# Optimization experiments

Hardware: AMD Instinct MI355X
Metric: run time of the kernel (lower is better)

The kernel has to match this reference:

```python
import jax, jax.numpy as jnp
import numpy as np

B, N_ATOMS, D_ATOM = 64, 256, 256
T_ANGLES = 2048
D_HID, D_OUT = 512, 256
BN_EPS = 1e-5


def setup_inputs() -> dict:
    key = jax.random.key(0)
    ks = jax.random.split(key, 8)
    z = jax.random.normal(ks[0], (B, N_ATOMS, D_ATOM), dtype=jnp.float32)
    # all entries valid (>=0) so the nonzero-selected row set is all B*T rows
    angel_atom_table = jax.random.randint(ks[1], (B, T_ANGLES, 3), 0, N_ATOMS, dtype=jnp.int64)
    W1 = jax.random.normal(ks[2], (D_ATOM, D_HID), dtype=jnp.float32) * (1.0 / np.sqrt(D_ATOM))
    b1 = jax.random.normal(ks[3], (D_HID,), dtype=jnp.float32) * 0.01
    gamma = jnp.ones((D_HID,), dtype=jnp.float32)
    beta = jnp.zeros((D_HID,), dtype=jnp.float32)
    W2 = jax.random.normal(ks[4], (D_HID, D_OUT), dtype=jnp.float32) * (1.0 / np.sqrt(D_HID))
    b2 = jax.random.normal(ks[5], (D_OUT,), dtype=jnp.float32) * 0.01
    return {"z": z, "angel_atom_table": angel_atom_table, "W1": W1, "b1": b1,
            "gamma": gamma, "beta": beta, "W2": W2, "b2": b2}


def reference(z, angel_atom_table, W1, b1, gamma, beta, W2, b2):
    Bb, Tt, _ = angel_atom_table.shape
    bi = jnp.arange(Bb)[:, None]                       # [B,1] broadcast batch index
    # gather 3 atom embeddings per angle and sum -> [B,T,d_atom]
    x = (z[bi, angel_atom_table[:, :, 0]]
         + z[bi, angel_atom_table[:, :, 1]]
         + z[bi, angel_atom_table[:, :, 2]])
    x = x.reshape(Bb * Tt, -1)                         # flattened valid rows (all valid)
    h = x @ W1 + b1                                    # Linear(d_atom, d_hid)
    mean = jnp.mean(h, axis=0)                         # BatchNorm1d (batch stats)
    var = jnp.var(h, axis=0)
    h = (h - mean) * jax.lax.rsqrt(var + BN_EPS) * gamma + beta
    h = jax.nn.relu(h)                                 # dropout inactive (eval)
    out = h @ W2 + b2                                  # Linear(d_hid, d_output)
    return out
```

## Files before the change

kernel.cpp:

```cpp
#include <hip/hip_runtime.h>

static constexpr int Bn  = 64;
static constexpr int T   = 2048;
static constexpr int NA  = 256;
static constexpr int DA  = 256;
static constexpr int DH  = 512;
static constexpr int DO  = 256;
static constexpr int M   = Bn * T;
static constexpr int NBS = M / 128;
static constexpr int NBC = M / 64;

typedef __attribute__((ext_vector_type(4))) float  f32x4;
typedef __attribute__((ext_vector_type(8))) __bf16 bf16x8;
typedef __attribute__((ext_vector_type(8))) short  short8;

__device__ __forceinline__ unsigned short f2bf(float f) {
  union { float f; unsigned u; } v; v.f = f;
  unsigned u = v.u + 0x7FFFu + ((v.u >> 16) & 1u);
  return (unsigned short)(u >> 16);
}
__device__ __forceinline__ float bf2f(unsigned short b) {
  union { unsigned u; float f; } v; v.u = ((unsigned)b) << 16;
  return v.f;
}

__global__ void prep_kernel(const float* __restrict__ W1, const float* __restrict__ W2,
                            unsigned short* __restrict__ W1T, unsigned short* __restrict__ W2T) {
  int id = blockIdx.x * 256 + threadIdx.x;
  {
    int n = id >> 8, k = id & 255;
    W1T[id] = f2bf(W1[k * DH + n]);
  }
  {
    int n = id >> 9, k = id & 511;
    W2T[id] = f2bf(W2[k * DO + n]);
  }
}

__global__ __launch_bounds__(512, 4) void kA_zw(
    const float* __restrict__ z, const unsigned short* __restrict__ W1T,
    unsigned short* __restrict__ zW) {
  __shared__ __align__(16) unsigned short As[32][64][8];
  const int tid = threadIdx.x;
  const int xcd = blockIdx.x & 7, idx = blockIdx.x >> 3;
  const int bm = xcd * 32 + (idx >> 1), bn = idx & 1;
  const int row0 = bm * 64, n0b = bn * 256;
  const int wave = tid >> 6, lane = tid & 63, ql = lane >> 4, r16 = lane & 15;
  const int gq = tid >> 8, t8 = tid & 255;
  const int gr = t8 >> 2, sub = t8 & 3;
  const int sxw = (sub << 2) ^ sub;
  const int sxr = (ql << 2) ^ ql;

  const unsigned short* bp = W1T + (size_t)(n0b + wave * 32 + r16) * DA + ql * 8;

  bf16x8 bq[2][2];
#pragma unroll
  for (int p = 0; p < 2; ++p)
#pragma unroll
    for (int nf = 0; nf < 2; ++nf)
      bq[p][nf] = *(const bf16x8*)(bp + nf * 16 * DA + p * 32);

  {
    const float* zr = z + (size_t)(row0 + gr) * DA + sub * 8;
#pragma unroll
    for (int cl = 0; cl < 4; ++cl) {
      const int cg = gq * 4 + cl;
      f32x4 a0 = *(const f32x4*)(zr + cg * 32);
      f32x4 a1 = *(const f32x4*)(zr + cg * 32 + 4);
      bf16x8 pk;
#pragma unroll
      for (int j = 0; j < 4; ++j) { pk[j] = (__bf16)a0[j]; pk[4 + j] = (__bf16)a1[j]; }
      *(bf16x8*)&As[cg * 4 + sub][gr ^ sxw][0] = pk;
    }
  }
  __syncthreads();

  f32x4 acc[4][2] = {};
#pragma unroll
  for (int s = 0; s < 8; ++s) {
    bf16x8 afr[4], bfr[2];
#pragma unroll
    for (int mf = 0; mf < 4; ++mf)
      afr[mf] = *(const bf16x8*)&As[s * 4 + ql][(mf * 16 + r16) ^ sxr][0];
#pragma unroll
    for (int nf = 0; nf < 2; ++nf) bfr[nf] = bq[s & 1][nf];
    __builtin_amdgcn_s_setprio(1);
#pragma unroll
    for (int mf = 0; mf < 4; ++mf)
#pragma unroll
      for (int nf = 0; nf < 2; ++nf)
        acc[mf][nf] = __builtin_amdgcn_mfma_f32_16x16x32_bf16(afr[mf], bfr[nf], acc[mf][nf], 0, 0, 0);
    __builtin_amdgcn_s_setprio(0);
    if (s + 2 < 8) {
#pragma unroll
      for (int nf = 0; nf < 2; ++nf)
        bq[s & 1][nf] = *(const bf16x8*)(bp + nf * 16 * DA + (s + 2) * 32);
    }
  }

  const int n0 = n0b + wave * 32;
#pragma unroll
  for (int nf = 0; nf < 2; ++nf) {
    const int col = n0 + nf * 16 + r16;
#pragma unroll
    for (int mf = 0; mf < 4; ++mf)
#pragma unroll
      for (int p = 0; p < 4; ++p)
        zW[(size_t)(row0 + mf * 16 + ql * 4 + p) * DH + col] = f2bf(acc[mf][nf][p]);
  }
}

__global__ __launch_bounds__(256) void kB_stats(
    const unsigned short* __restrict__ zW, const int* __restrict__ tbl,
    float* __restrict__ psum, float* __restrict__ psq) {
  __shared__ int idxs[128][3];
  __shared__ float red1[4][512];
  __shared__ float red2[4][512];
  const int bid = blockIdx.x;
  const int blk = (bid & 7) * (NBS >> 3) + (bid >> 3);
  const int tid = threadIdx.x;
  const int row0 = blk * 128;
  const unsigned short* zWb = zW + (size_t)(row0 >> 11) * NA * DH;

  for (int i = tid; i < 384; i += 256) ((int*)idxs)[i] = tbl[(size_t)row0 * 3 + i];
  __syncthreads();

  const int cc = tid & 63, rg = tid >> 6;
  float s1[8] = {0, 0, 0, 0, 0, 0, 0, 0};
  float s2[8] = {0, 0, 0, 0, 0, 0, 0, 0};
#pragma unroll 8
  for (int i = 0; i < 32; ++i) {
    const int r = rg * 32 + i;
    const unsigned short* p0 = zWb + (size_t)idxs[r][0] * DH + cc * 8;
    const unsigned short* p1 = zWb + (size_t)idxs[r][1] * DH + cc * 8;
    const unsigned short* p2 = zWb + (size_t)idxs[r][2] * DH + cc * 8;
    short8 v0 = *(const short8*)p0;
    short8 v1 = *(const short8*)p1;
    short8 v2 = *(const short8*)p2;
#pragma unroll
    for (int j = 0; j < 8; ++j) {
      float h = bf2f((unsigned short)v0[j]) + bf2f((unsigned short)v1[j]) + bf2f((unsigned short)v2[j]);
      s1[j] += h;
      s2[j] = fmaf(h, h, s2[j]);
    }
  }
#pragma unroll
  for (int j = 0; j < 8; ++j) { red1[rg][cc * 8 + j] = s1[j]; red2[rg][cc * 8 + j] = s2[j]; }
  __syncthreads();
  for (int c = tid; c < 512; c += 256) {
    psum[(size_t)c * NBS + blk] = red1[0][c] + red1[1][c] + red1[2][c] + red1[3][c];
    psq [(size_t)c * NBS + blk] = red2[0][c] + red2[1][c] + red2[2][c] + red2[3][c];
  }
}

__global__ void k2_stats(const float* __restrict__ psum, const float* __restrict__ psq,
                         const float* __restrict__ gamma, const float* __restrict__ beta,
                         float* __restrict__ coef) {
  const int col = blockIdx.x, lane = threadIdx.x;
  float s1 = 0.f, s2 = 0.f;
  for (int i = lane; i < NBS; i += 64) {
    s1 += psum[(size_t)col * NBS + i];
    s2 += psq [(size_t)col * NBS + i];
  }
#pragma unroll
  for (int d = 1; d < 64; d <<= 1) { s1 += __shfl_xor(s1, d); s2 += __shfl_xor(s2, d); }
  if (lane == 0) {
    const float inv = 1.0f / (float)M;
    float mean = s1 * inv;
    float var  = s2 * inv - mean * mean;
    float a = gamma[col] * rsqrtf(var + 1e-5f);
    coef[col]      = a;
    coef[DH + col] = beta[col] - mean * a;
  }
}

__global__ __launch_bounds__(512, 4) void kC_out(
    const unsigned short* __restrict__ zW, const int* __restrict__ tbl,
    const unsigned short* __restrict__ W2T, const float* __restrict__ coef,
    const float* __restrict__ b2, float* __restrict__ out) {
  __shared__ __align__(16) unsigned short As[32][64][8];
  __shared__ float aC[DH], dC[DH];
  __shared__ int idxs[64][3];

  const int bid = blockIdx.x;
  const int blk = (bid & 7) * (NBC >> 3) + (bid >> 3);
  const int tid = threadIdx.x;
  const int row0 = blk * 64;
  const unsigned short* zWb = zW + (size_t)(row0 >> 11) * NA * DH;

  if (tid < 192) ((int*)idxs)[tid] = tbl[(size_t)row0 * 3 + tid];
  aC[tid] = coef[tid];
  dC[tid] = coef[DH + tid];
  __syncthreads();

  const int wave = tid >> 6, lane = tid & 63, ql = lane >> 4, r16 = lane & 15;
  const int gq = tid >> 8, t8 = tid & 255;
  const int gr = t8 >> 2, sub = t8 & 3;
  const int sxw = (sub << 2) ^ sub;
  const int sxr = (ql << 2) ^ ql;

  const unsigned short* g0p = zWb + (size_t)idxs[gr][0] * DH + sub * 8;
  const unsigned short* g1p = zWb + (size_t)idxs[gr][1] * DH + sub * 8;
  const unsigned short* g2p = zWb + (size_t)idxs[gr][2] * DH + sub * 8;

  const unsigned short* bp = W2T + (size_t)(wave * 32 + r16) * DH + ql * 8;

  bf16x8 bq[2][2];
#pragma unroll
  for (int p = 0; p < 2; ++p)
#pragma unroll
    for (int nf = 0; nf < 2; ++nf)
      bq[p][nf] = *(const bf16x8*)(bp + nf * 16 * DH + p * 32);

  f32x4 acc[4][2] = {};

#pragma unroll
  for (int h = 0; h < 2; ++h) {
    if (h) __builtin_amdgcn_s_barrier();
#pragma unroll
    for (int cl = 0; cl < 4; ++cl) {
      const int coff = h * 256 + (gq * 4 + cl) * 32;
      short8 v0 = *(const short8*)(g0p + coff);
      short8 v1 = *(const short8*)(g1p + coff);
      short8 v2 = *(const short8*)(g2p + coff);
      const int kk = coff + sub * 8;
      f32x4 av0 = *(const f32x4*)&aC[kk];
      f32x4 av1 = *(const f32x4*)&aC[kk + 4];
      f32x4 dv0 = *(const f32x4*)&dC[kk];
      f32x4 dv1 = *(const f32x4*)&dC[kk + 4];
      bf16x8 pk;
#pragma unroll
      for (int j = 0; j < 4; ++j) {
        float h0 = bf2f((unsigned short)v0[j]) + bf2f((unsigned short)v1[j]) + bf2f((unsigned short)v2[j]);
        float f0 = fmaf(h0, av0[j], dv0[j]);
        f0 = f0 > 0.f ? f0 : 0.f;
        pk[j] = (__bf16)f0;
        float h1 = bf2f((unsigned short)v0[4 + j]) + bf2f((unsigned short)v1[4 + j]) + bf2f((unsigned short)v2[4 + j]);
        float f1 = fmaf(h1, av1[j], dv1[j]);
        f1 = f1 > 0.f ? f1 : 0.f;
        pk[4 + j] = (__bf16)f1;
      }
      *(bf16x8*)&As[(gq * 4 + cl) * 4 + sub][gr ^ sxw][0] = pk;
    }
    asm volatile("s_waitcnt lgkmcnt(0)" ::: "memory");
    __builtin_amdgcn_s_barrier();
    __builtin_amdgcn_sched_barrier(0);

#pragma unroll
    for (int s = 0; s < 8; ++s) {
      const int sg = h * 8 + s;
      bf16x8 afr[4], bfr[2];
#pragma unroll
      for (int mf = 0; mf < 4; ++mf)
        afr[mf] = *(const bf16x8*)&As[s * 4 + ql][(mf * 16 + r16) ^ sxr][0];
#pragma unroll
      for (int nf = 0; nf < 2; ++nf) bfr[nf] = bq[sg & 1][nf];
      __builtin_amdgcn_s_setprio(1);
#pragma unroll
      for (int mf = 0; mf < 4; ++mf)
#pragma unroll
        for (int nf = 0; nf < 2; ++nf)
          acc[mf][nf] = __builtin_amdgcn_mfma_f32_16x16x32_bf16(afr[mf], bfr[nf], acc[mf][nf], 0, 0, 0);
      __builtin_amdgcn_s_setprio(0);
      if (sg + 2 < 16) {
#pragma unroll
        for (int nf = 0; nf < 2; ++nf)
          bq[sg & 1][nf] = *(const bf16x8*)(bp + nf * 16 * DH + (sg + 2) * 32);
      }
    }
  }

  const int n0 = wave * 32;
#pragma unroll
  for (int nf = 0; nf < 2; ++nf) {
    const int col = n0 + nf * 16 + r16;
    const float bv = b2[col];
#pragma unroll
    for (int mf = 0; mf < 4; ++mf)
#pragma unroll
      for (int p = 0; p < 4; ++p)
        out[(size_t)(row0 + mf * 16 + ql * 4 + p) * DO + col] = acc[mf][nf][p] + bv;
  }
}

extern "C" void kernel_launch(void* const* d_in, const int* in_sizes, int n_in,
                              void* d_out, int out_size, void* d_ws, size_t ws_size,
                              hipStream_t stream) {
  const float* z     = (const float*)d_in[0];
  const int*   tbl   = (const int*)d_in[1];
  const float* W1    = (const float*)d_in[2];
  const float* gamma = (const float*)d_in[4];
  const float* beta  = (const float*)d_in[5];
  const float* W2    = (const float*)d_in[6];
  const float* b2    = (const float*)d_in[7];
  float* out = (float*)d_out;

  char* ws = (char*)d_ws;
  unsigned short* W1T  = (unsigned short*)(ws);
  unsigned short* W2T  = (unsigned short*)(ws + (256 << 10));
  float*          coef = (float*)(ws + (512 << 10));
  float*          psum = (float*)(ws + (2 << 20));
  float*          psq  = (float*)(ws + (4 << 20));
  unsigned short* zW   = (unsigned short*)(ws + (16 << 20));

  prep_kernel<<<512, 256, 0, stream>>>(W1, W2, W1T, W2T);
  kA_zw<<<512, 512, 0, stream>>>(z, W1T, zW);
  kB_stats<<<NBS, 256, 0, stream>>>(zW, tbl, psum, psq);
  k2_stats<<<DH, 64, 0, stream>>>(psum, psq, gamma, beta, coef);
  kC_out<<<NBC, 512, 0, stream>>>(zW, tbl, W2T, coef, b2, out);
}
```

Measured before the change: 268.5 us.

## Prefetch gathered rows into registers and overlap second-half gather with MFMA

```diff
diff --git a/kernel.cpp b/kernel.cpp
--- a/kernel.cpp
+++ b/kernel.cpp
@@ -180,7 +180,6 @@
     const float* __restrict__ b2, float* __restrict__ out) {
   __shared__ __align__(16) unsigned short As[32][64][8];
   __shared__ float aC[DH], dC[DH];
-  __shared__ int idxs[64][3];
 
   const int bid = blockIdx.x;
   const int blk = (bid & 7) * (NBC >> 3) + (bid >> 3);
@@ -188,98 +187,160 @@
   const int row0 = blk * 64;
   const unsigned short* zWb = zW + (size_t)(row0 >> 11) * NA * DH;
 
-  if (tid < 192) ((int*)idxs)[tid] = tbl[(size_t)row0 * 3 + tid];
   aC[tid] = coef[tid];
   dC[tid] = coef[DH + tid];
+
+  const int gr = tid >> 3, sc = tid & 7;
+  const size_t tb = (size_t)(row0 + gr) * 3;
+  const int i0 = tbl[tb], i1 = tbl[tb + 1], i2 = tbl[tb + 2];
+  const unsigned short* g0p = zWb + (size_t)i0 * DH + sc * 8;
+  const unsigned short* g1p = zWb + (size_t)i1 * DH + sc * 8;
+  const unsigned short* g2p = zWb + (size_t)i2 * DH + sc * 8;
+
+  short8 a0[4], a1[4], a2[4];
+#pragma unroll
+  for (int it = 0; it < 4; ++it) {
+    a0[it] = *(const short8*)(g0p + it * 64);
+    a1[it] = *(const short8*)(g1p + it * 64);
+    a2[it] = *(const short8*)(g2p + it * 64);
+  }
+
+  const int wave = tid >> 6, lane = tid & 63, ql = lane >> 4, r16 = lane & 15;
+  const int rg2 = wave >> 2;
+  const int cg  = wave & 3;
+
+  const unsigned short* bp = W2T + (size_t)(cg * 64 + r16) * DH + ql * 8;
+  bf16x8 bq[2][4];
+#pragma unroll
+  for (int p = 0; p < 2; ++p)
+#pragma unroll
+    for (int nf = 0; nf < 4; ++nf)
+      bq[p][nf] = *(const bf16x8*)(bp + nf * 16 * DH + p * 32);
+
   __syncthreads();
 
-  const int wave = tid >> 6, lane = tid & 63, ql = lane >> 4, r16 = lane & 15;
-  const int gq = tid >> 8, t8 = tid & 255;
-  const int gr = t8 >> 2, sub = t8 & 3;
-  const int sxw = (sub << 2) ^ sub;
-  const int sxr = (ql << 2) ^ ql;
-
-  const unsigned short* g0p = zWb + (size_t)idxs[gr][0] * DH + sub * 8;
-  const unsigned short* g1p = zWb + (size_t)idxs[gr][1] * DH + sub * 8;
-  const unsigned short* g2p = zWb + (size_t)idxs[gr][2] * DH + sub * 8;
-
-  const unsigned short* bp = W2T + (size_t)(wave * 32 + r16) * DH + ql * 8;
-
-  bf16x8 bq[2][2];
-#pragma unroll
-  for (int p = 0; p < 2; ++p)
-#pragma unroll
-    for (int nf = 0; nf < 2; ++nf)
-      bq[p][nf] = *(const bf16x8*)(bp + nf * 16 * DH + p * 32);
-
-  f32x4 acc[4][2] = {};
-
-#pragma unroll
-  for (int h = 0; h < 2; ++h) {
-    if (h) __builtin_amdgcn_s_barrier();
-#pragma unroll
-    for (int cl = 0; cl < 4; ++cl) {
-      const int coff = h * 256 + (gq * 4 + cl) * 32;
-      short8 v0 = *(const short8*)(g0p + coff);
-      short8 v1 = *(const short8*)(g1p + coff);
-      short8 v2 = *(const short8*)(g2p + coff);
-      const int kk = coff + sub * 8;
-      f32x4 av0 = *(const f32x4*)&aC[kk];
-      f32x4 av1 = *(const f32x4*)&aC[kk + 4];
-      f32x4 dv0 = *(const f32x4*)&dC[kk];
-      f32x4 dv1 = *(const f32x4*)&dC[kk + 4];
-      bf16x8 pk;
-#pragma unroll
-      for (int j = 0; j < 4; ++j) {
-        float h0 = bf2f((unsigned short)v0[j]) + bf2f((unsigned short)v1[j]) + bf2f((unsigned short)v2[j]);
-        float f0 = fmaf(h0, av0[j], dv0[j]);
-        f0 = f0 > 0.f ? f0 : 0.f;
-        pk[j] = (__bf16)f0;
-        float h1 = bf2f((unsigned short)v0[4 + j]) + bf2f((unsigned short)v1[4 + j]) + bf2f((unsigned short)v2[4 + j]);
-        float f1 = fmaf(h1, av1[j], dv1[j]);
-        f1 = f1 > 0.f ? f1 : 0.f;
-        pk[4 + j] = (__bf16)f1;
-      }
-      *(bf16x8*)&As[(gq * 4 + cl) * 4 + sub][gr ^ sxw][0] = pk;
-    }
-    asm volatile("s_waitcnt lgkmcnt(0)" ::: "memory");
-    __builtin_amdgcn_s_barrier();
-    __builtin_amdgcn_sched_barrier(0);
-
-#pragma unroll
-    for (int s = 0; s < 8; ++s) {
-      const int sg = h * 8 + s;
-      bf16x8 afr[4], bfr[2];
-#pragma unroll
-      for (int mf = 0; mf < 4; ++mf)
-        afr[mf] = *(const bf16x8*)&As[s * 4 + ql][(mf * 16 + r16) ^ sxr][0];
-#pragma unroll
-      for (int nf = 0; nf < 2; ++nf) bfr[nf] = bq[sg & 1][nf];
-      __builtin_amdgcn_s_setprio(1);
-#pragma unroll
-      for (int mf = 0; mf < 4; ++mf)
-#pragma unroll
-        for (int nf = 0; nf < 2; ++nf)
-          acc[mf][nf] = __builtin_amdgcn_mfma_f32_16x16x32_bf16(afr[mf], bfr[nf], acc[mf][nf], 0, 0, 0);
-      __builtin_amdgcn_s_setprio(0);
-      if (sg + 2 < 16) {
-#pragma unroll
-        for (int nf = 0; nf < 2; ++nf)
-          bq[sg & 1][nf] = *(const bf16x8*)(bp + nf * 16 * DH + (sg + 2) * 32);
-      }
-    }
-  }
-
-  const int n0 = wave * 32;
-#pragma unroll
-  for (int nf = 0; nf < 2; ++nf) {
-    const int col = n0 + nf * 16 + r16;
+#pragma unroll
+  for (int it = 0; it < 4; ++it) {
+    const int kk = it * 64 + sc * 8;
+    f32x4 av0 = *(const f32x4*)&aC[kk];
+    f32x4 av1 = *(const f32x4*)&aC[kk + 4];
+    f32x4 dv0 = *(const f32x4*)&dC[kk];
+    f32x4 dv1 = *(const f32x4*)&dC[kk + 4];
+    bf16x8 pk;
+#pragma unroll
+    for (int j = 0; j < 4; ++j) {
+      float h0 = bf2f((unsigned short)a0[it][j]) + bf2f((unsigned short)a1[it][j]) + bf2f((unsigned short)a2[it][j]);
+      float f0 = fmaf(h0, av0[j], dv0[j]);
+      f0 = f0 > 0.f ? f0 : 0.f;
+      pk[j] = (__bf16)f0;
+      float h1 = bf2f((unsigned short)a0[it][4 + j]) + bf2f((unsigned short)a1[it][4 + j]) + bf2f((unsigned short)a2[it][4 + j]);
+      float f1 = fmaf(h1, av1[j], dv1[j]);
+      f1 = f1 > 0.f ? f1 : 0.f;
+      pk[4 + j] = (__bf16)f1;
+    }
+    *(bf16x8*)&As[it * 8 + sc][gr ^ sc][0] = pk;
+  }
+
+  short8 p0[4], p1[4];
+#pragma unroll
+  for (int it = 0; it < 4; ++it) {
+    p0[it] = *(const short8*)(g0p + 256 + it * 64);
+    p1[it] = *(const short8*)(g1p + 256 + it * 64);
+  }
+
+  asm volatile("s_waitcnt lgkmcnt(0)" ::: "memory");
+  __builtin_amdgcn_s_barrier();
+  __builtin_amdgcn_sched_barrier(0);
+
+  f32x4 acc[2][4] = {};
+
+#pragma unroll
+  for (int s = 0; s < 8; ++s) {
+    const int swz = ((s & 1) << 2) | ql;
+    bf16x8 afr[2], bfr[4];
+#pragma unroll
+    for (int mf = 0; mf < 2; ++mf)
+      afr[mf] = *(const bf16x8*)&As[s * 4 + ql][(rg2 * 32 + mf * 16 + r16) ^ swz][0];
+#pragma unroll
+    for (int nf = 0; nf < 4; ++nf) bfr[nf] = bq[s & 1][nf];
+    __builtin_amdgcn_s_setprio(1);
+#pragma unroll
+    for (int mf = 0; mf < 2; ++mf)
+#pragma unroll
+      for (int nf = 0; nf < 4; ++nf)
+        acc[mf][nf] = __builtin_amdgcn_mfma_f32_16x16x32_bf16(afr[mf], bfr[nf], acc[mf][nf], 0, 0, 0);
+    __builtin_amdgcn_s_setprio(0);
+#pragma unroll
+    for (int nf = 0; nf < 4; ++nf)
+      bq[s & 1][nf] = *(const bf16x8*)(bp + nf * 16 * DH + (s + 2) * 32);
+  }
+
+  __builtin_amdgcn_s_barrier();
+
+  short8 p2[4];
+#pragma unroll
+  for (int it = 0; it < 4; ++it)
+    p2[it] = *(const short8*)(g2p + 256 + it * 64);
+
+#pragma unroll
+  for (int it = 0; it < 4; ++it) {
+    const int kk = 256 + it * 64 + sc * 8;
+    f32x4 av0 = *(const f32x4*)&aC[kk];
+    f32x4 av1 = *(const f32x4*)&aC[kk + 4];
+    f32x4 dv0 = *(const f32x4*)&dC[kk];
+    f32x4 dv1 = *(const f32x4*)&dC[kk + 4];
+    bf16x8 pk;
+#pragma unroll
+    for (int j = 0; j < 4; ++j) {
+      float h0 = bf2f((unsigned short)p0[it][j]) + bf2f((unsigned short)p1[it][j]) + bf2f((unsigned short)p2[it][j]);
+      float f0 = fmaf(h0, av0[j], dv0[j]);
+      f0 = f0 > 0.f ? f0 : 0.f;
+      pk[j] = (__bf16)f0;
+      float h1 = bf2f((unsigned short)p0[it][4 + j]) + bf2f((unsigned short)p1[it][4 + j]) + bf2f((unsigned short)p2[it][4 + j]);
+      float f1 = fmaf(h1, av1[j], dv1[j]);
+      f1 = f1 > 0.f ? f1 : 0.f;
+      pk[4 + j] = (__bf16)f1;
+    }
+    *(bf16x8*)&As[it * 8 + sc][gr ^ sc][0] = pk;
+  }
+  asm volatile("s_waitcnt lgkmcnt(0)" ::: "memory");
+  __builtin_amdgcn_s_barrier();
+  __builtin_amdgcn_sched_barrier(0);
+
+#pragma unroll
+  for (int s = 0; s < 8; ++s) {
+    const int sg = 8 + s;
+    const int swz = ((s & 1) << 2) | ql;
+    bf16x8 afr[2], bfr[4];
+#pragma unroll
+    for (int mf = 0; mf < 2; ++mf)
+      afr[mf] = *(const bf16x8*)&As[s * 4 + ql][(rg2 * 32 + mf * 16 + r16) ^ swz][0];
+#pragma unroll
+    for (int nf = 0; nf < 4; ++nf) bfr[nf] = bq[sg & 1][nf];
+    __builtin_amdgcn_s_setprio(1);
+#pragma unroll
+    for (int mf = 0; mf < 2; ++mf)
+#pragma unroll
+      for (int nf = 0; nf < 4; ++nf)
+        acc[mf][nf] = __builtin_amdgcn_mfma_f32_16x16x32_bf16(afr[mf], bfr[nf], acc[mf][nf], 0, 0, 0);
+    __builtin_amdgcn_s_setprio(0);
+    if (sg + 2 < 16) {
+#pragma unroll
+      for (int nf = 0; nf < 4; ++nf)
+        bq[sg & 1][nf] = *(const bf16x8*)(bp + nf * 16 * DH + (sg + 2) * 32);
+    }
+  }
+
+  const int c0 = cg * 64, r0w = row0 + rg2 * 32;
+#pragma unroll
+  for (int nf = 0; nf < 4; ++nf) {
+    const int col = c0 + nf * 16 + r16;
     const float bv = b2[col];
 #pragma unroll
-    for (int mf = 0; mf < 4; ++mf)
+    for (int mf = 0; mf < 2; ++mf)
 #pragma unroll
       for (int p = 0; p < 4; ++p)
-        out[(size_t)(row0 + mf * 16 + ql * 4 + p) * DO + col] = acc[mf][nf][p] + bv;
+        out[(size_t)(r0w + mf * 16 + ql * 4 + p) * DO + col] = acc[mf][nf][p] + bv;
   }
 }
 
```

After: 337.9 us. 25.9% more time.
